# Performance work log

Hardware: AMD Instinct MI355X
Metric: run time of the kernel (lower is better)

The kernel has to match this reference:

```python
import jax, jax.numpy as jnp
import numpy as np

EMBED_DIM = 1024
SHIFT = 0.0

def setup_inputs() -> dict:
    key = jax.random.key(0)
    k1, k2, k3 = jax.random.split(key, 3)
    inputs = jax.random.normal(k1, (4, 2048, EMBED_DIM), dtype=jnp.float32)
    rotation_params = jax.random.normal(k2, (EMBED_DIM, EMBED_DIM), dtype=jnp.float32)
    entangle_params = jax.random.normal(k3, (EMBED_DIM, EMBED_DIM), dtype=jnp.float32)
    return {"inputs": inputs, "rotation_params": rotation_params, "entangle_params": entangle_params}

def reference(inputs, rotation_params, entangle_params):
    # inputs: (b, s, d)
    d = inputs.shape[-1]
    query = jnp.einsum('bsd,de->bse', inputs, rotation_params)
    key = jnp.einsum('bsd,de->bse', inputs, entangle_params)
    scores = jax.nn.softmax(jnp.einsum('bqd,bkd->bqk', query, key) / np.sqrt(d), axis=-1)
    out = jnp.einsum('bqk,bkd->bqd', scores, inputs)
    return jax.nn.sigmoid(out + SHIFT)
```

## Files before the change

### kernel.cpp

```cpp
#include <hip/hip_runtime.h>
#include <hip/hip_bf16.h>
#include <math.h>


using u16 = unsigned short;
using short8 = __attribute__((ext_vector_type(8))) short;
using f32x4  = __attribute__((ext_vector_type(4))) float;

__device__ static inline u16 f2bf(float f) {
    union { __hip_bfloat16 h; u16 u; } cv; cv.h = __float2bfloat16(f); return cv.u;
}
__device__ static inline float bf2f(u16 u) {
    union { __hip_bfloat16 h; u16 u; } cv; cv.u = u; return __bfloat162float(cv.h);
}
__device__ static inline void split2(float v, u16& h, u16& l) {
    h = f2bf(v);
    l = f2bf(v - bf2f(h));
}

__device__ static inline void gload16(const u16* g, u16* l) {
    __builtin_amdgcn_global_load_lds(
        (const __attribute__((address_space(1))) void*)g,
        (__attribute__((address_space(3))) void*)l, 16, 0, 0);
}

__device__ static inline short8 ldfrag(const u16* sm, int row, int g) {
    const int off = row * 32 + ((g ^ ((row >> 1) & 3)) << 3);
    return *reinterpret_cast<const short8*>(sm + off);
}

enum { EP_F32 = 0, EP_HILO = 1, EP_SIG = 2 };

template<int EPI, bool TRIPLE>
__global__ __launch_bounds__(256)
void gemm_split(const u16* __restrict__ Ahi, const u16* __restrict__ Alo,
                const u16* __restrict__ Bhi, const u16* __restrict__ Blo,
                float* __restrict__ Cf, u16* __restrict__ Chi, u16* __restrict__ Clo,
                int K, int lda, int ldb, int ldc,
                long sA, long sB, long sC, float alpha)
{
    const int z = blockIdx.z;
    Ahi += z * sA;
    Bhi += z * sB;
    if (TRIPLE) { Alo += z * sA; Blo += z * sB; }
    if (EPI == EP_HILO) { Chi += z * sC; Clo += z * sC; }
    else                { Cf  += z * sC; }

    constexpr int NTILE = TRIPLE ? 4 : 2;
    __shared__ __align__(16) u16 smem[NTILE * 4096];
    u16* lAh = &smem[0];
    u16* lBh = &smem[TRIPLE ? 8192 : 4096];
    u16* lAl = TRIPLE ? &smem[4096]  : nullptr;
    u16* lBl = TRIPLE ? &smem[12288] : nullptr;

    const int t = threadIdx.x;
    const int wave = t >> 6, lane = t & 63;
    const int row0 = blockIdx.y * 128, col0 = blockIdx.x * 128;

    const int rr = t >> 2, cc = t & 3;
    const int gg = cc ^ ((rr >> 1) & 3);
    const long aoff0 = (long)(row0 + rr) * lda + gg * 8;
    const long aoff1 = (long)(row0 + 64 + rr) * lda + gg * 8;
    const long boff0 = (long)(col0 + rr) * ldb + gg * 8;
    const long boff1 = (long)(col0 + 64 + rr) * ldb + gg * 8;
    const int ldsW = wave * 512;

    f32x4 acc[4][4];
    #pragma unroll
    for (int m = 0; m < 4; m++)
        #pragma unroll
        for (int n = 0; n < 4; n++)
            acc[m][n] = (f32x4){0.f, 0.f, 0.f, 0.f};

    const int lr = lane & 15, lg = lane >> 4;
    const int wm = (wave >> 1) * 64, wn = (wave & 1) * 64;

    for (int k0 = 0; k0 < K; k0 += 32) {
        gload16(Ahi + aoff0 + k0, lAh + 0 * 2048 + ldsW);
        gload16(Ahi + aoff1 + k0, lAh + 1 * 2048 + ldsW);
        gload16(Bhi + boff0 + k0, lBh + 0 * 2048 + ldsW);
        gload16(Bhi + boff1 + k0, lBh + 1 * 2048 + ldsW);
        if (TRIPLE) {
            gload16(Alo + aoff0 + k0, lAl + 0 * 2048 + ldsW);
            gload16(Alo + aoff1 + k0, lAl + 1 * 2048 + ldsW);
            gload16(Blo + boff0 + k0, lBl + 0 * 2048 + ldsW);
            gload16(Blo + boff1 + k0, lBl + 1 * 2048 + ldsW);
        }
        __syncthreads();

        short8 ah[4], al[4];
        #pragma unroll
        for (int m = 0; m < 4; m++) {
            ah[m] = ldfrag(lAh, wm + m * 16 + lr, lg);
            if (TRIPLE) al[m] = ldfrag(lAl, wm + m * 16 + lr, lg);
        }
        #pragma unroll
        for (int n = 0; n < 4; n++) {
            const short8 bh = ldfrag(lBh, wn + n * 16 + lr, lg);
            short8 bl;
            if (TRIPLE) bl = ldfrag(lBl, wn + n * 16 + lr, lg);
            #pragma unroll
            for (int m = 0; m < 4; m++) {
                acc[m][n] = __builtin_amdgcn_mfma_f32_16x16x32_bf16(ah[m], bh, acc[m][n], 0, 0, 0);
                if (TRIPLE) {
                    acc[m][n] = __builtin_amdgcn_mfma_f32_16x16x32_bf16(ah[m], bl, acc[m][n], 0, 0, 0);
                    acc[m][n] = __builtin_amdgcn_mfma_f32_16x16x32_bf16(al[m], bh, acc[m][n], 0, 0, 0);
                }
            }
        }
        __syncthreads();
    }

    #pragma unroll
    for (int m = 0; m < 4; m++) {
        #pragma unroll
        for (int n = 0; n < 4; n++) {
            #pragma unroll
            for (int r = 0; r < 4; r++) {
                const int grow = row0 + wm + m * 16 + lg * 4 + r;
                const int gcol = col0 + wn + n * 16 + lr;
                const float v = alpha * acc[m][n][r];
                const long o = (long)grow * ldc + gcol;
                if (EPI == EP_F32) {
                    Cf[o] = v;
                } else if (EPI == EP_SIG) {
                    Cf[o] = 1.0f / (1.0f + __expf(-v));
                } else {
                    u16 h, l; split2(v, h, l);
                    Chi[o] = h; Clo[o] = l;
                }
            }
        }
    }
}

__global__ __launch_bounds__(256)
void split_rm(const float* __restrict__ in, u16* __restrict__ hi, u16* __restrict__ lo)
{
    const long i = ((long)blockIdx.x * 256 + threadIdx.x) * 4;
    const float4 v = *reinterpret_cast<const float4*>(in + i);
    ushort4 h, l;
    split2(v.x, h.x, l.x);
    split2(v.y, h.y, l.y);
    split2(v.z, h.z, l.z);
    split2(v.w, h.w, l.w);
    *reinterpret_cast<ushort4*>(hi + i) = h;
    *reinterpret_cast<ushort4*>(lo + i) = l;
}

__global__ __launch_bounds__(256)
void reduce4_split(const float* __restrict__ p, u16* __restrict__ hi, u16* __restrict__ lo,
                   long n)
{
    const long i = ((long)blockIdx.x * 256 + threadIdx.x) * 4;
    const float4 a = *reinterpret_cast<const float4*>(p + i);
    const float4 b = *reinterpret_cast<const float4*>(p + n + i);
    const float4 c = *reinterpret_cast<const float4*>(p + 2 * n + i);
    const float4 d = *reinterpret_cast<const float4*>(p + 3 * n + i);
    ushort4 h, l;
    split2((a.x + b.x) + (c.x + d.x), h.x, l.x);
    split2((a.y + b.y) + (c.y + d.y), h.y, l.y);
    split2((a.z + b.z) + (c.z + d.z), h.z, l.z);
    split2((a.w + b.w) + (c.w + d.w), h.w, l.w);
    *reinterpret_cast<ushort4*>(hi + i) = h;
    *reinterpret_cast<ushort4*>(lo + i) = l;
}

template<bool HILO>
__global__ __launch_bounds__(256)
void split_tr(const float* __restrict__ in, u16* __restrict__ hi, u16* __restrict__ lo,
              int R, int C, long sIn, long sOut)
{
    in += (long)blockIdx.z * sIn;
    hi += (long)blockIdx.z * sOut;
    if (HILO) lo += (long)blockIdx.z * sOut;

    __shared__ float tile[32][33];
    const int tx = threadIdx.x & 31, ty = threadIdx.x >> 5;
    const int r0 = blockIdx.y * 32, c0 = blockIdx.x * 32;

    #pragma unroll
    for (int j = 0; j < 4; j++)
        tile[ty * 4 + j][tx] = in[(long)(r0 + ty * 4 + j) * C + c0 + tx];
    __syncthreads();

    #pragma unroll
    for (int j = 0; j < 4; j++) {
        const int oc = ty * 4 + j;
        const float v = tile[tx][oc];
        u16 h, l; split2(v, h, l);
        const long o = (long)(c0 + oc) * R + r0 + tx;
        hi[o] = h;
        if (HILO) lo[o] = l;
    }
}

__global__ __launch_bounds__(256)
void softmax_hi(const float* __restrict__ S, u16* __restrict__ hi)
{
    const int NC = 2048;
    const long base = (long)blockIdx.x * NC;
    const float* p = S + base;
    const int tid = threadIdx.x;

    float4 v0 = reinterpret_cast<const float4*>(p)[tid];
    float4 v1 = reinterpret_cast<const float4*>(p)[tid + 256];

    float m = fmaxf(fmaxf(fmaxf(v0.x, v0.y), fmaxf(v0.z, v0.w)),
                    fmaxf(fmaxf(v1.x, v1.y), fmaxf(v1.z, v1.w)));
    #pragma unroll
    for (int off = 1; off < 64; off <<= 1)
        m = fmaxf(m, __shfl_xor(m, off));

    __shared__ float redm[4];
    __shared__ float reds[4];
    const int wave = tid >> 6, lane = tid & 63;
    if (lane == 0) redm[wave] = m;
    __syncthreads();
    m = fmaxf(fmaxf(redm[0], redm[1]), fmaxf(redm[2], redm[3]));

    v0.x = __expf(v0.x - m); v0.y = __expf(v0.y - m);
    v0.z = __expf(v0.z - m); v0.w = __expf(v0.w - m);
    v1.x = __expf(v1.x - m); v1.y = __expf(v1.y - m);
    v1.z = __expf(v1.z - m); v1.w = __expf(v1.w - m);

    float s = (v0.x + v0.y + v0.z + v0.w) + (v1.x + v1.y + v1.z + v1.w);
    #pragma unroll
    for (int off = 1; off < 64; off <<= 1)
        s += __shfl_xor(s, off);
    if (lane == 0) reds[wave] = s;
    __syncthreads();
    s = (reds[0] + reds[1]) + (reds[2] + reds[3]);

    const float inv = 1.0f / s;
    ushort4 h0, h1;
    h0.x = f2bf(v0.x * inv); h0.y = f2bf(v0.y * inv);
    h0.z = f2bf(v0.z * inv); h0.w = f2bf(v0.w * inv);
    h1.x = f2bf(v1.x * inv); h1.y = f2bf(v1.y * inv);
    h1.z = f2bf(v1.z * inv); h1.w = f2bf(v1.w * inv);

    reinterpret_cast<ushort4*>(hi + base)[tid]       = h0;
    reinterpret_cast<ushort4*>(hi + base)[tid + 256] = h1;
}

extern "C" void kernel_launch(void* const* d_in, const int* in_sizes, int n_in,
                              void* d_out, int out_size, void* d_ws, size_t ws_size,
                              hipStream_t stream)
{
    (void)in_sizes; (void)n_in; (void)out_size; (void)ws_size;
    const float* X = (const float*)d_in[0];
    const float* R = (const float*)d_in[1];
    const float* E = (const float*)d_in[2];
    float* out = (float*)d_out;

    const int B = 4, SQ = 2048, D = 1024;
    const long NDX = (long)B * SQ * D;
    const long DD  = (long)D * D;
    const long SS  = (long)B * SQ * SQ;
    const long M16 = 8388608;

    u16* wsu = (u16*)d_ws;
    u16* Xhi  = wsu;
    u16* Xlo  = Xhi + NDX;
    u16* Rhi  = wsu + 2 * M16;
    u16* Rlo  = Rhi + DD;
    u16* Ehi  = Rlo + DD;
    u16* Elo  = Ehi + DD;
    u16* Yhi  = wsu + 2 * M16;
    u16* Ylo  = Yhi + NDX;
    u16* Shi  = wsu + 2 * M16;
    u16* Xthi = wsu;
    float* Wpart = (float*)(wsu + 4 * M16);
    u16* Wthi = wsu + 5 * M16;
    u16* Wtlo = Wthi + DD;
    float* Sf = (float*)(wsu + 4 * M16);

    dim3 thr(256);

    split_rm<<<dim3((unsigned)(NDX / 1024)), thr, 0, stream>>>(X, Xhi, Xlo);
    split_rm<<<dim3((unsigned)(DD / 1024)), thr, 0, stream>>>(R, Rhi, Rlo);
    split_rm<<<dim3((unsigned)(DD / 1024)), thr, 0, stream>>>(E, Ehi, Elo);

    gemm_split<EP_F32, true><<<dim3(D / 128, D / 128, 4), thr, 0, stream>>>(
        Ehi, Elo, Rhi, Rlo, Wpart, nullptr, nullptr,
        256, D, D, D, 256, 256, DD, 1.0f);
    reduce4_split<<<dim3((unsigned)(DD / 1024)), thr, 0, stream>>>(Wpart, Wthi, Wtlo, DD);

    gemm_split<EP_HILO, true><<<dim3(D / 128, (B * SQ) / 128, 1), thr, 0, stream>>>(
        Xhi, Xlo, Wthi, Wtlo, nullptr, Yhi, Ylo,
        D, D, D, D, 0, 0, 0, 1.0f);

    gemm_split<EP_F32, true><<<dim3(SQ / 128, SQ / 128, B), thr, 0, stream>>>(
        Yhi, Ylo, Xhi, Xlo, Sf, nullptr, nullptr,
        D, D, D, SQ,
        (long)SQ * D, (long)SQ * D, (long)SQ * SQ, 0.03125f);

    softmax_hi<<<dim3(B * SQ), thr, 0, stream>>>(Sf, Shi);

    split_tr<false><<<dim3(D / 32, SQ / 32, B), thr, 0, stream>>>(
        X, Xthi, nullptr, SQ, D, (long)SQ * D, (long)SQ * D);

    gemm_split<EP_SIG, false><<<dim3(D / 128, SQ / 128, B), thr, 0, stream>>>(
        Shi, nullptr, Xthi, nullptr, out, nullptr, nullptr,
        SQ, SQ, SQ, D,
        (long)SQ * SQ, (long)SQ * D, (long)SQ * D, 1.0f);
}
```

Baseline: 290.4 us.

## Add 256x256 ping-pong pipelined triple-bf16 GEMM for attention scores

Adds a new 512-thread kernel for the Y·Xᵀ score GEMM. It uses 256x256 output tiles with double-buffered LDS and splits each K-step into four phases, interleaving fragment loads, async global-to-LDS prefetch and MFMA bursts under barriers and raised wave priority. The larger tile raises data reuse per load and the phased schedule aims to hide memory latency behind the triple-bf16 MFMAs. In exchange it needs 128KB of LDS and many accumulator registers, which limits occupancy to one block per CU, and it assumes dimensions divisible by 256.

```diff
diff --git a/kernel.cpp b/kernel.cpp
--- a/kernel.cpp
+++ b/kernel.cpp
@@ -6,6 +6,8 @@
 using u16 = unsigned short;
 using short8 = __attribute__((ext_vector_type(8))) short;
 using f32x4  = __attribute__((ext_vector_type(4))) float;
+
+#define MFB(a, b, c) __builtin_amdgcn_mfma_f32_16x16x32_bf16((a), (b), (c), 0, 0, 0)
 
 __device__ static inline u16 f2bf(float f) {
     union { __hip_bfloat16 h; u16 u; } cv; cv.h = __float2bfloat16(f); return cv.u;
@@ -101,10 +103,10 @@
             if (TRIPLE) bl = ldfrag(lBl, wn + n * 16 + lr, lg);
             #pragma unroll
             for (int m = 0; m < 4; m++) {
-                acc[m][n] = __builtin_amdgcn_mfma_f32_16x16x32_bf16(ah[m], bh, acc[m][n], 0, 0, 0);
+                acc[m][n] = MFB(ah[m], bh, acc[m][n]);
                 if (TRIPLE) {
-                    acc[m][n] = __builtin_amdgcn_mfma_f32_16x16x32_bf16(ah[m], bl, acc[m][n], 0, 0, 0);
-                    acc[m][n] = __builtin_amdgcn_mfma_f32_16x16x32_bf16(al[m], bh, acc[m][n], 0, 0, 0);
+                    acc[m][n] = MFB(ah[m], bl, acc[m][n]);
+                    acc[m][n] = MFB(al[m], bh, acc[m][n]);
                 }
             }
         }
@@ -129,6 +131,169 @@
                     u16 h, l; split2(v, h, l);
                     Chi[o] = h; Clo[o] = l;
                 }
+            }
+        }
+    }
+}
+
+__global__ __launch_bounds__(512)
+void gemm_triple_8ph(const u16* __restrict__ Ahi, const u16* __restrict__ Alo,
+                     const u16* __restrict__ Bhi, const u16* __restrict__ Blo,
+                     float* __restrict__ Cf,
+                     int K, int lda, int ldb, int ldc,
+                     long sA, long sB, long sC, float alpha)
+{
+    const int z = blockIdx.z;
+    Ahi += z * sA; Alo += z * sA;
+    Bhi += z * sB; Blo += z * sB;
+    Cf  += z * sC;
+
+    __shared__ __align__(16) u16 smem[65536];
+
+    const int t = threadIdx.x;
+    const int wave = t >> 6, lane = t & 63;
+    const int lr = lane & 15, lg = lane >> 4;
+    const int row0 = blockIdx.y * 256, col0 = blockIdx.x * 256;
+    const int wm = (wave >> 2) * 128, wn = (wave & 3) * 64;
+
+    const int srow = t >> 2;
+    const int sg = (t & 3) ^ ((srow >> 1) & 3);
+    const u16* gAh = Ahi + (long)(row0 + srow) * lda + sg * 8;
+    const u16* gAl = Alo + (long)(row0 + srow) * lda + sg * 8;
+    const u16* gBh = Bhi + (long)(col0 + srow) * ldb + sg * 8;
+    const u16* gBl = Blo + (long)(col0 + srow) * ldb + sg * 8;
+    const long a2 = (long)128 * lda, b2 = (long)128 * ldb;
+
+    f32x4 acc[8][4];
+    #pragma unroll
+    for (int m = 0; m < 8; m++)
+        #pragma unroll
+        for (int n = 0; n < 4; n++)
+            acc[m][n] = (f32x4){0.f, 0.f, 0.f, 0.f};
+
+    const int NT = K >> 5;
+
+    {
+        u16* d = smem + t * 8;
+        gload16(gAh,      d);          gload16(gAh + a2, d + 4096);
+        gload16(gAl,      d + 8192);   gload16(gAl + a2, d + 12288);
+        gload16(gBh,      d + 16384);  gload16(gBh + b2, d + 20480);
+        gload16(gBl,      d + 24576);  gload16(gBl + b2, d + 28672);
+    }
+
+    short8 ah[4], al[4], bh[2], bl[2];
+
+    for (int tk = 0; tk < NT; ++tk) {
+        const int cur = tk & 1;
+        const u16* sAh = smem + cur * 32768;
+        const u16* sAl = sAh + 8192;
+        const u16* sBh = sAh + 16384;
+        const u16* sBl = sAh + 24576;
+        const bool pf = (tk + 1 < NT);
+        const int kn = (tk + 1) << 5;
+        u16* d = smem + (cur ^ 1) * 32768 + t * 8;
+
+        asm volatile("s_waitcnt vmcnt(0)" ::: "memory");
+        __builtin_amdgcn_s_barrier();
+
+        #pragma unroll
+        for (int mm = 0; mm < 4; mm++) {
+            ah[mm] = ldfrag(sAh, wm + mm * 16 + lr, lg);
+            al[mm] = ldfrag(sAl, wm + mm * 16 + lr, lg);
+        }
+        #pragma unroll
+        for (int nn = 0; nn < 2; nn++) {
+            bh[nn] = ldfrag(sBh, wn + nn * 16 + lr, lg);
+            bl[nn] = ldfrag(sBl, wn + nn * 16 + lr, lg);
+        }
+        if (pf) {
+            gload16(gAh + kn,      d);
+            gload16(gAh + kn + a2, d + 4096);
+            gload16(gAl + kn,      d + 8192);
+            gload16(gAl + kn + a2, d + 12288);
+        }
+        __builtin_amdgcn_s_barrier();
+        __builtin_amdgcn_s_setprio(1);
+        #pragma unroll
+        for (int nn = 0; nn < 2; nn++)
+            #pragma unroll
+            for (int mm = 0; mm < 4; mm++) {
+                acc[mm][nn] = MFB(ah[mm], bh[nn], acc[mm][nn]);
+                acc[mm][nn] = MFB(ah[mm], bl[nn], acc[mm][nn]);
+                acc[mm][nn] = MFB(al[mm], bh[nn], acc[mm][nn]);
+            }
+        __builtin_amdgcn_s_setprio(0);
+        __builtin_amdgcn_s_barrier();
+
+        #pragma unroll
+        for (int nn = 0; nn < 2; nn++) {
+            bh[nn] = ldfrag(sBh, wn + (2 + nn) * 16 + lr, lg);
+            bl[nn] = ldfrag(sBl, wn + (2 + nn) * 16 + lr, lg);
+        }
+        if (pf) {
+            gload16(gBh + kn,      d + 16384);
+            gload16(gBh + kn + b2, d + 20480);
+            gload16(gBl + kn,      d + 24576);
+            gload16(gBl + kn + b2, d + 28672);
+        }
+        __builtin_amdgcn_s_barrier();
+        __builtin_amdgcn_s_setprio(1);
+        #pragma unroll
+        for (int nn = 0; nn < 2; nn++)
+            #pragma unroll
+            for (int mm = 0; mm < 4; mm++) {
+                acc[mm][2 + nn] = MFB(ah[mm], bh[nn], acc[mm][2 + nn]);
+                acc[mm][2 + nn] = MFB(ah[mm], bl[nn], acc[mm][2 + nn]);
+                acc[mm][2 + nn] = MFB(al[mm], bh[nn], acc[mm][2 + nn]);
+            }
+        __builtin_amdgcn_s_setprio(0);
+        __builtin_amdgcn_s_barrier();
+
+        #pragma unroll
+        for (int mm = 0; mm < 4; mm++) {
+            ah[mm] = ldfrag(sAh, wm + (4 + mm) * 16 + lr, lg);
+            al[mm] = ldfrag(sAl, wm + (4 + mm) * 16 + lr, lg);
+        }
+        __builtin_amdgcn_s_barrier();
+        __builtin_amdgcn_s_setprio(1);
+        #pragma unroll
+        for (int nn = 0; nn < 2; nn++)
+            #pragma unroll
+            for (int mm = 0; mm < 4; mm++) {
+                acc[4 + mm][2 + nn] = MFB(ah[mm], bh[nn], acc[4 + mm][2 + nn]);
+                acc[4 + mm][2 + nn] = MFB(ah[mm], bl[nn], acc[4 + mm][2 + nn]);
+                acc[4 + mm][2 + nn] = MFB(al[mm], bh[nn], acc[4 + mm][2 + nn]);
+            }
+        __builtin_amdgcn_s_setprio(0);
+        __builtin_amdgcn_s_barrier();
+
+        #pragma unroll
+        for (int nn = 0; nn < 2; nn++) {
+            bh[nn] = ldfrag(sBh, wn + nn * 16 + lr, lg);
+            bl[nn] = ldfrag(sBl, wn + nn * 16 + lr, lg);
+        }
+        __builtin_amdgcn_s_barrier();
+        __builtin_amdgcn_s_setprio(1);
+        #pragma unroll
+        for (int nn = 0; nn < 2; nn++)
+            #pragma unroll
+            for (int mm = 0; mm < 4; mm++) {
+                acc[4 + mm][nn] = MFB(ah[mm], bh[nn], acc[4 + mm][nn]);
+                acc[4 + mm][nn] = MFB(ah[mm], bl[nn], acc[4 + mm][nn]);
+                acc[4 + mm][nn] = MFB(al[mm], bh[nn], acc[4 + mm][nn]);
+            }
+        __builtin_amdgcn_s_setprio(0);
+    }
+
+    #pragma unroll
+    for (int m = 0; m < 8; m++) {
+        #pragma unroll
+        for (int n = 0; n < 4; n++) {
+            #pragma unroll
+            for (int r = 0; r < 4; r++) {
+                const int grow = row0 + wm + m * 16 + lg * 4 + r;
+                const int gcol = col0 + wn + n * 16 + lr;
+                Cf[(long)grow * ldc + gcol] = alpha * acc[m][n][r];
             }
         }
     }
@@ -290,8 +455,8 @@
         Xhi, Xlo, Wthi, Wtlo, nullptr, Yhi, Ylo,
         D, D, D, D, 0, 0, 0, 1.0f);
 
-    gemm_split<EP_F32, true><<<dim3(SQ / 128, SQ / 128, B), thr, 0, stream>>>(
-        Yhi, Ylo, Xhi, Xlo, Sf, nullptr, nullptr,
+    gemm_triple_8ph<<<dim3(SQ / 256, SQ / 256, B), dim3(512), 0, stream>>>(
+        Yhi, Ylo, Xhi, Xlo, Sf,
         D, D, D, SQ,
         (long)SQ * D, (long)SQ * D, (long)SQ * SQ, 0.03125f);
 
```

Result: faster. 273.6 us (-5.8%).

## Double-buffer LDS in split GEMMs and add 256x256 tile triple-bf16 score GEMM

Applied to the files above, without the earlier changes.

The generic split-bf16 GEMM now double-buffers its LDS tiles: it prefetches the next K-slice with async global-to-LDS loads while computing the current one, and it drops the trailing barrier. A new 512-thread kernel with 256x256 tiles computes the QK^T score GEMM, giving more reuse per loaded element. The cost is twice the LDS use, with 128 KB per block in the new kernel, and higher register pressure from 32 accumulator tiles. Both reduce occupancy.

```diff
diff --git a/kernel.cpp b/kernel.cpp
--- a/kernel.cpp
+++ b/kernel.cpp
@@ -6,6 +6,8 @@
 using u16 = unsigned short;
 using short8 = __attribute__((ext_vector_type(8))) short;
 using f32x4  = __attribute__((ext_vector_type(4))) float;
+
+#define MFB(a, b, c) __builtin_amdgcn_mfma_f32_16x16x32_bf16((a), (b), (c), 0, 0, 0)
 
 __device__ static inline u16 f2bf(float f) {
     union { __hip_bfloat16 h; u16 u; } cv; cv.h = __float2bfloat16(f); return cv.u;
@@ -46,12 +48,9 @@
     if (EPI == EP_HILO) { Chi += z * sC; Clo += z * sC; }
     else                { Cf  += z * sC; }
 
-    constexpr int NTILE = TRIPLE ? 4 : 2;
-    __shared__ __align__(16) u16 smem[NTILE * 4096];
-    u16* lAh = &smem[0];
-    u16* lBh = &smem[TRIPLE ? 8192 : 4096];
-    u16* lAl = TRIPLE ? &smem[4096]  : nullptr;
-    u16* lBl = TRIPLE ? &smem[12288] : nullptr;
+    constexpr int BUFSZ  = TRIPLE ? 16384 : 8192;
+    constexpr int OFF_BH = TRIPLE ? 8192 : 4096;
+    __shared__ __align__(16) u16 smem[2 * BUFSZ];
 
     const int t = threadIdx.x;
     const int wave = t >> 6, lane = t & 63;
@@ -59,11 +58,11 @@
 
     const int rr = t >> 2, cc = t & 3;
     const int gg = cc ^ ((rr >> 1) & 3);
-    const long aoff0 = (long)(row0 + rr) * lda + gg * 8;
-    const long aoff1 = (long)(row0 + 64 + rr) * lda + gg * 8;
-    const long boff0 = (long)(col0 + rr) * ldb + gg * 8;
-    const long boff1 = (long)(col0 + 64 + rr) * ldb + gg * 8;
-    const int ldsW = wave * 512;
+    const u16* gAh = Ahi + (long)(row0 + rr) * lda + gg * 8;
+    const u16* gBh = Bhi + (long)(col0 + rr) * ldb + gg * 8;
+    const u16* gAl = TRIPLE ? (Alo + (long)(row0 + rr) * lda + gg * 8) : nullptr;
+    const u16* gBl = TRIPLE ? (Blo + (long)(col0 + rr) * ldb + gg * 8) : nullptr;
+    const long a2 = (long)64 * lda, b2 = (long)64 * ldb;
 
     f32x4 acc[4][4];
     #pragma unroll
@@ -74,41 +73,64 @@
 
     const int lr = lane & 15, lg = lane >> 4;
     const int wm = (wave >> 1) * 64, wn = (wave & 1) * 64;
-
-    for (int k0 = 0; k0 < K; k0 += 32) {
-        gload16(Ahi + aoff0 + k0, lAh + 0 * 2048 + ldsW);
-        gload16(Ahi + aoff1 + k0, lAh + 1 * 2048 + ldsW);
-        gload16(Bhi + boff0 + k0, lBh + 0 * 2048 + ldsW);
-        gload16(Bhi + boff1 + k0, lBh + 1 * 2048 + ldsW);
+    const int NT = K >> 5;
+
+    {
+        u16* d = smem + t * 8;
+        gload16(gAh,      d);
+        gload16(gAh + a2, d + 2048);
+        gload16(gBh,      d + OFF_BH);
+        gload16(gBh + b2, d + OFF_BH + 2048);
         if (TRIPLE) {
-            gload16(Alo + aoff0 + k0, lAl + 0 * 2048 + ldsW);
-            gload16(Alo + aoff1 + k0, lAl + 1 * 2048 + ldsW);
-            gload16(Blo + boff0 + k0, lBl + 0 * 2048 + ldsW);
-            gload16(Blo + boff1 + k0, lBl + 1 * 2048 + ldsW);
-        }
+            gload16(gAl,      d + 4096);
+            gload16(gAl + a2, d + 4096 + 2048);
+            gload16(gBl,      d + 12288);
+            gload16(gBl + b2, d + 12288 + 2048);
+        }
+    }
+
+    for (int tk = 0; tk < NT; ++tk) {
         __syncthreads();
-
-        short8 ah[4], al[4];
+        const u16* sb = smem + (tk & 1) * BUFSZ;
+        if (tk + 1 < NT) {
+            const int kn = (tk + 1) << 5;
+            u16* d = smem + ((tk + 1) & 1) * BUFSZ + t * 8;
+            gload16(gAh + kn,      d);
+            gload16(gAh + kn + a2, d + 2048);
+            gload16(gBh + kn,      d + OFF_BH);
+            gload16(gBh + kn + b2, d + OFF_BH + 2048);
+            if (TRIPLE) {
+                gload16(gAl + kn,      d + 4096);
+                gload16(gAl + kn + a2, d + 4096 + 2048);
+                gload16(gBl + kn,      d + 12288);
+                gload16(gBl + kn + b2, d + 12288 + 2048);
+            }
+        }
+        const u16* sAh = sb;
+        const u16* sAl = sb + 4096;
+        const u16* sBh = sb + OFF_BH;
+        const u16* sBl = sb + 12288;
+
+        short8 bh[4], bl[4];
+        #pragma unroll
+        for (int n = 0; n < 4; n++) {
+            bh[n] = ldfrag(sBh, wn + n * 16 + lr, lg);
+            if (TRIPLE) bl[n] = ldfrag(sBl, wn + n * 16 + lr, lg);
+        }
         #pragma unroll
         for (int m = 0; m < 4; m++) {
-            ah[m] = ldfrag(lAh, wm + m * 16 + lr, lg);
-            if (TRIPLE) al[m] = ldfrag(lAl, wm + m * 16 + lr, lg);
-        }
-        #pragma unroll
-        for (int n = 0; n < 4; n++) {
-            const short8 bh = ldfrag(lBh, wn + n * 16 + lr, lg);
-            short8 bl;
-            if (TRIPLE) bl = ldfrag(lBl, wn + n * 16 + lr, lg);
+            const short8 ah = ldfrag(sAh, wm + m * 16 + lr, lg);
+            short8 al;
+            if (TRIPLE) al = ldfrag(sAl, wm + m * 16 + lr, lg);
             #pragma unroll
-            for (int m = 0; m < 4; m++) {
-                acc[m][n] = __builtin_amdgcn_mfma_f32_16x16x32_bf16(ah[m], bh, acc[m][n], 0, 0, 0);
+            for (int n = 0; n < 4; n++) {
+                acc[m][n] = MFB(ah, bh[n], acc[m][n]);
                 if (TRIPLE) {
-                    acc[m][n] = __builtin_amdgcn_mfma_f32_16x16x32_bf16(ah[m], bl, acc[m][n], 0, 0, 0);
-                    acc[m][n] = __builtin_amdgcn_mfma_f32_16x16x32_bf16(al[m], bh, acc[m][n], 0, 0, 0);
+                    acc[m][n] = MFB(ah, bl[n], acc[m][n]);
+                    acc[m][n] = MFB(al, bh[n], acc[m][n]);
                 }
             }
         }
-        __syncthreads();
     }
 
     #pragma unroll
@@ -134,6 +156,100 @@
     }
 }
 
+__global__ __launch_bounds__(512)
+void gemm_triple_256(const u16* __restrict__ Ahi, const u16* __restrict__ Alo,
+                     const u16* __restrict__ Bhi, const u16* __restrict__ Blo,
+                     float* __restrict__ Cf,
+                     int K, int lda, int ldb, int ldc,
+                     long sA, long sB, long sC, float alpha)
+{
+    const int z = blockIdx.z;
+    Ahi += z * sA; Alo += z * sA;
+    Bhi += z * sB; Blo += z * sB;
+    Cf  += z * sC;
+
+    __shared__ __align__(16) u16 smem[65536];
+
+    const int t = threadIdx.x;
+    const int wave = t >> 6, lane = t & 63;
+    const int lr = lane & 15, lg = lane >> 4;
+    const int row0 = blockIdx.y * 256, col0 = blockIdx.x * 256;
+    const int wm = (wave >> 2) * 128, wn = (wave & 3) * 64;
+
+    const int srow = t >> 2;
+    const int sg = (t & 3) ^ ((srow >> 1) & 3);
+    const u16* gAh = Ahi + (long)(row0 + srow) * lda + sg * 8;
+    const u16* gAl = Alo + (long)(row0 + srow) * lda + sg * 8;
+    const u16* gBh = Bhi + (long)(col0 + srow) * ldb + sg * 8;
+    const u16* gBl = Blo + (long)(col0 + srow) * ldb + sg * 8;
+    const long a2 = (long)128 * lda, b2 = (long)128 * ldb;
+
+    f32x4 acc[8][4];
+    #pragma unroll
+    for (int m = 0; m < 8; m++)
+        #pragma unroll
+        for (int n = 0; n < 4; n++)
+            acc[m][n] = (f32x4){0.f, 0.f, 0.f, 0.f};
+
+    const int NT = K >> 5;
+
+    {
+        u16* d = smem + t * 8;
+        gload16(gAh,      d);          gload16(gAh + a2, d + 4096);
+        gload16(gAl,      d + 8192);   gload16(gAl + a2, d + 12288);
+        gload16(gBh,      d + 16384);  gload16(gBh + b2, d + 20480);
+        gload16(gBl,      d + 24576);  gload16(gBl + b2, d + 28672);
+    }
+
+    for (int tk = 0; tk < NT; ++tk) {
+        __syncthreads();
+        const u16* sb = smem + (tk & 1) * 32768;
+        if (tk + 1 < NT) {
+            const int kn = (tk + 1) << 5;
+            u16* d = smem + ((tk + 1) & 1) * 32768 + t * 8;
+            gload16(gAh + kn,      d);          gload16(gAh + kn + a2, d + 4096);
+            gload16(gAl + kn,      d + 8192);   gload16(gAl + kn + a2, d + 12288);
+            gload16(gBh + kn,      d + 16384);  gload16(gBh + kn + b2, d + 20480);
+            gload16(gBl + kn,      d + 24576);  gload16(gBl + kn + b2, d + 28672);
+        }
+        const u16* sAh = sb;
+        const u16* sAl = sb + 8192;
+        const u16* sBh = sb + 16384;
+        const u16* sBl = sb + 24576;
+
+        short8 bh[4], bl[4];
+        #pragma unroll
+        for (int n = 0; n < 4; n++) {
+            bh[n] = ldfrag(sBh, wn + n * 16 + lr, lg);
+            bl[n] = ldfrag(sBl, wn + n * 16 + lr, lg);
+        }
+        #pragma unroll
+        for (int m = 0; m < 8; m++) {
+            const short8 ah = ldfrag(sAh, wm + m * 16 + lr, lg);
+            const short8 al = ldfrag(sAl, wm + m * 16 + lr, lg);
+            #pragma unroll
+            for (int n = 0; n < 4; n++) {
+                acc[m][n] = MFB(ah, bh[n], acc[m][n]);
+                acc[m][n] = MFB(ah, bl[n], acc[m][n]);
+                acc[m][n] = MFB(al, bh[n], acc[m][n]);
+            }
+        }
+    }
+
+    #pragma unroll
+    for (int m = 0; m < 8; m++) {
+        #pragma unroll
+        for (int n = 0; n < 4; n++) {
+            #pragma unroll
+            for (int r = 0; r < 4; r++) {
+                const int grow = row0 + wm + m * 16 + lg * 4 + r;
+                const int gcol = col0 + wn + n * 16 + lr;
+                Cf[(long)grow * ldc + gcol] = alpha * acc[m][n][r];
+            }
+        }
+    }
+}
+
 __global__ __launch_bounds__(256)
 void split_rm(const float* __restrict__ in, u16* __restrict__ hi, u16* __restrict__ lo)
 {
@@ -290,8 +406,8 @@
         Xhi, Xlo, Wthi, Wtlo, nullptr, Yhi, Ylo,
         D, D, D, D, 0, 0, 0, 1.0f);
 
-    gemm_split<EP_F32, true><<<dim3(SQ / 128, SQ / 128, B), thr, 0, stream>>>(
-        Yhi, Ylo, Xhi, Xlo, Sf, nullptr, nullptr,
+    gemm_triple_256<<<dim3(SQ / 256, SQ / 256, B), dim3(512), 0, stream>>>(
+        Yhi, Ylo, Xhi, Xlo, Sf,
         D, D, D, SQ,
         (long)SQ * D, (long)SQ * D, (long)SQ * SQ, 0.03125f);
 
```

Result: faster. 251.1 us (-13.5%).
